# Optimization experiments

Hardware: AMD Instinct MI355X
Metric: run time of the kernel (lower is better)

The kernel has to match this reference:

```python
import jax, jax.numpy as jnp
import numpy as np

HEADS = 12
DIM_HEAD = 64
SCALE = DIM_HEAD ** -0.5


def setup_inputs() -> dict:
    key = jax.random.key(0)
    ks = jax.random.split(key, 5)
    b, n, dim = 16, 1024, 768
    inner = HEADS * DIM_HEAD  # 768
    x = jax.random.normal(ks[0], (b, n, dim), dtype=jnp.float32)
    w_qv = jax.random.normal(ks[1], (dim, 2 * inner), dtype=jnp.float32) * (dim ** -0.5)
    ext_k = jax.random.normal(ks[2], (1, HEADS, n, DIM_HEAD), dtype=jnp.float32)
    ext_bias = jax.random.normal(ks[3], (1, HEADS, n, n), dtype=jnp.float32)
    w_out = jax.random.normal(ks[4], (inner, dim), dtype=jnp.float32) * (inner ** -0.5)
    b_out = jnp.zeros((dim,), dtype=jnp.float32)
    return {"x": x, "w_qv": w_qv, "ext_k": ext_k, "ext_bias": ext_bias,
            "w_out": w_out, "b_out": b_out}


def reference(x, w_qv, ext_k, ext_bias, w_out, b_out):
    b, n, _ = x.shape
    qv = x @ w_qv                                   # [b, n, 2*inner]
    q, v = jnp.split(qv, 2, axis=-1)
    # b n (h d) -> b h n d
    q = q.reshape(b, n, HEADS, DIM_HEAD).transpose(0, 2, 1, 3)
    v = v.reshape(b, n, HEADS, DIM_HEAD).transpose(0, 2, 1, 3)
    # dots = (q @ ext_k^T + ext_bias) * scale       # [b, h, n, n]
    dots = (jnp.einsum('bhnd,ohmd->bhnm', q, ext_k) + ext_bias) * SCALE
    attn = jax.nn.softmax(dots, axis=-1)
    out = jnp.einsum('bhnm,bhmd->bhnd', attn, v)    # [b, h, n, d]
    out = out.transpose(0, 2, 1, 3).reshape(b, n, HEADS * DIM_HEAD)
    return out @ w_out + b_out
```

## Files before the change

kernel.cpp:

```cpp
#include <hip/hip_runtime.h>
#include <hip/hip_bf16.h>
#include <stdint.h>

typedef __bf16 bf16;
typedef short  s16x8 __attribute__((ext_vector_type(8)));
typedef float  f32x4 __attribute__((ext_vector_type(4)));

#define NHEADS  12
#define QKSCALE 0.125f

__device__ __forceinline__ void gload_lds16(const void* g, void* l) {
  __builtin_amdgcn_global_load_lds(
      (__attribute__((address_space(1))) void*)(g),
      (__attribute__((address_space(3))) void*)(l), 16, 0, 0);
}

__device__ __forceinline__ short bf16bits(float f) {
  union { bf16 h; short s; } u;
  u.h = (bf16)f;
  return u.s;
}
__device__ __forceinline__ float bfu2f(unsigned short u) {
  union { unsigned int i; float f; } c;
  c.i = ((unsigned int)u) << 16;
  return c.f;
}

__global__ __launch_bounds__(256) void cast4_kernel(const float* __restrict__ in,
                                                    bf16* __restrict__ out,
                                                    int n4, float scale) {
  int i = blockIdx.x * 256 + threadIdx.x;
  if (i >= n4) return;
  float4 v = ((const float4*)in)[i];
  union { bf16 h[4]; uint64_t u; } o;
  o.h[0] = (bf16)(v.x * scale);
  o.h[1] = (bf16)(v.y * scale);
  o.h[2] = (bf16)(v.z * scale);
  o.h[3] = (bf16)(v.w * scale);
  ((uint64_t*)out)[i] = o.u;
}

__global__ __launch_bounds__(256) void castT_tiled(const float* __restrict__ in,
                                                   bf16* __restrict__ out,
                                                   int R, int C) {
  __shared__ float tile[32][33];
  const int nbx = C >> 5;
  const int bx = blockIdx.x % nbx, by = blockIdx.x / nbx;
  const int tx = threadIdx.x & 31, ty = threadIdx.x >> 5;
  const int r0 = by << 5, c0 = bx << 5;
#pragma unroll
  for (int i = 0; i < 4; ++i)
    tile[ty + i * 8][tx] = in[(size_t)(r0 + ty + i * 8) * C + c0 + tx];
  __syncthreads();
#pragma unroll
  for (int i = 0; i < 4; ++i)
    out[(size_t)(c0 + ty + i * 8) * R + r0 + tx] = (bf16)tile[tx][ty + i * 8];
}

template <int EPI>
__global__ __launch_bounds__(256) void gemm128(const bf16* __restrict__ A,
                                               const bf16* __restrict__ BT,
                                               int M, int N, int K,
                                               bf16* __restrict__ outQ,
                                               bf16* __restrict__ outVT,
                                               float* __restrict__ outC,
                                               const float* __restrict__ bias) {
  __shared__ char sA[2][8192];
  __shared__ char sB[2][8192];
  const int cpx = gridDim.x >> 3;
  const int orig = blockIdx.x;
  const int blk = (orig & 7) * cpx + (orig >> 3);
  const int nb = N >> 7;
  const int bx = blk % nb, by = blk / nb;
  const int brow = by << 7, bcol = bx << 7;
  const int t = threadIdx.x;
  const int w = t >> 6, l = t & 63;
  const int wr = w >> 1, wc = w & 1;
  const int lr = l & 15, lg = l >> 4;

  const f32x4 fz = {0.f, 0.f, 0.f, 0.f};
  f32x4 acc[4][4];
#pragma unroll
  for (int m = 0; m < 4; ++m)
#pragma unroll
    for (int n = 0; n < 4; ++n) acc[m][n] = fz;

#define G_STAGE(kt_, buf_)                                                     \
  {                                                                            \
    _Pragma("unroll") for (int i = 0; i < 2; ++i) {                            \
      int chunk = ((i * 4 + w) << 6) + l;                                      \
      int rrow = chunk >> 2, rc = chunk & 3;                                   \
      gload_lds16(A + (size_t)(brow + rrow) * K + ((kt_) << 5) + (rc << 3),    \
                  sA[buf_] + ((i * 4 + w) << 10));                             \
      gload_lds16(BT + (size_t)(bcol + rrow) * K + ((kt_) << 5) + (rc << 3),   \
                  sB[buf_] + ((i * 4 + w) << 10));                             \
    }                                                                          \
  }

  const int nk = K >> 5;
  G_STAGE(0, 0);
  __syncthreads();
  for (int kt = 0; kt < nk; ++kt) {
    const int cur = kt & 1, nxt = cur ^ 1;
    if (kt + 1 < nk) G_STAGE(kt + 1, nxt);
    s16x8 af[4], bfr[4];
#pragma unroll
    for (int m = 0; m < 4; ++m)
      af[m] = *(const s16x8*)(sA[cur] + ((wr << 6) + (m << 4) + lr) * 64 + (lg << 4));
#pragma unroll
    for (int n = 0; n < 4; ++n)
      bfr[n] = *(const s16x8*)(sB[cur] + ((wc << 6) + (n << 4) + lr) * 64 + (lg << 4));
    __builtin_amdgcn_s_setprio(1);
#pragma unroll
    for (int m = 0; m < 4; ++m)
#pragma unroll
      for (int n = 0; n < 4; ++n)
        acc[m][n] = __builtin_amdgcn_mfma_f32_16x16x32_bf16(af[m], bfr[n], acc[m][n], 0, 0, 0);
    __builtin_amdgcn_s_setprio(0);
    __syncthreads();
  }
#undef G_STAGE

  if (EPI == 0) {
#pragma unroll
    for (int n = 0; n < 4; ++n) {
      int gcol = bcol + (wc << 6) + (n << 4) + lr;
      if (gcol < 768) {
        int h = gcol >> 6, d = gcol & 63;
#pragma unroll
        for (int m = 0; m < 4; ++m) {
          int growb = brow + (wr << 6) + (m << 4) + (lg << 2);
#pragma unroll
          for (int r = 0; r < 4; ++r) {
            int grow = growb + r;
            int b = grow >> 10, nr = grow & 1023;
            outQ[(((size_t)(b * NHEADS + h) << 10) + nr) * 64 + d] =
                (bf16)(acc[m][n][r] * QKSCALE);
          }
        }
      } else {
        int c2 = gcol - 768;
        int h = c2 >> 6, d = c2 & 63;
#pragma unroll
        for (int m = 0; m < 4; ++m) {
          int growb = brow + (wr << 6) + (m << 4) + (lg << 2);
          int b = growb >> 10, nr0 = growb & 1023;
          ushort4 pk;
          pk.x = (unsigned short)bf16bits(acc[m][n][0]);
          pk.y = (unsigned short)bf16bits(acc[m][n][1]);
          pk.z = (unsigned short)bf16bits(acc[m][n][2]);
          pk.w = (unsigned short)bf16bits(acc[m][n][3]);
          *(ushort4*)(outVT + ((((size_t)(b * NHEADS + h) << 6) + d) << 10) + nr0) = pk;
        }
      }
    }
  } else {
#pragma unroll
    for (int n = 0; n < 4; ++n) {
      int gcol = bcol + (wc << 6) + (n << 4) + lr;
      float bv = bias[gcol];
#pragma unroll
      for (int m = 0; m < 4; ++m) {
        int growb = brow + (wr << 6) + (m << 4) + (lg << 2);
#pragma unroll
        for (int r = 0; r < 4; ++r)
          outC[(size_t)(growb + r) * N + gcol] = acc[m][n][r] + bv;
      }
    }
  }
}

__global__ __launch_bounds__(256) void attn_kernel(const bf16* __restrict__ Q,
                                                   const bf16* __restrict__ VT,
                                                   const bf16* __restrict__ Kx,
                                                   const bf16* __restrict__ Bias,
                                                   bf16* __restrict__ O) {
  __shared__ char sK[2][8192];
  __shared__ char sVT[2][8192];
  __shared__ char sP[4][4096];

  const int cpx = gridDim.x >> 3;
  const int orig = blockIdx.x;
  const int blk = (orig & 7) * cpx + (orig >> 3);

  const int b  = blk & 15;
  const int qb = (blk >> 4) & 7;
  const int h  = blk >> 7;
  const int bh = b * NHEADS + h;
  const int t = threadIdx.x, w = t >> 6, l = t & 63;
  const int lr = l & 15, lg = l >> 4;
  const int q0 = (qb << 7) + (w << 5);
  const size_t qvbase = (size_t)bh << 10;

  s16x8 qf[2][2];
#pragma unroll
  for (int qg = 0; qg < 2; ++qg)
#pragma unroll
    for (int kf = 0; kf < 2; ++kf)
      qf[qg][kf] = *(const s16x8*)(Q + ((qvbase + q0 + (qg << 4) + lr) << 6) +
                                   (kf << 5) + (lg << 3));

  const f32x4 fz = {0.f, 0.f, 0.f, 0.f};
  f32x4 acc_o[2][4];
#pragma unroll
  for (int qg = 0; qg < 2; ++qg)
#pragma unroll
    for (int of = 0; of < 4; ++of) acc_o[qg][of] = fz;
  float lsum[2] = {0.f, 0.f};

  const bf16* Kh = Kx + ((size_t)h << 16);
  const bf16* Brow0 = Bias + ((size_t)((h << 10) + q0 + lr)) * 1024;
  const bf16* Brow1 = Brow0 + (16 << 10);
  const bf16* Vth = VT + (qvbase << 6);

#define STAGE_K(kt_, buf_)                                                  \
  {                                                                         \
    _Pragma("unroll") for (int i = 0; i < 2; ++i) {                         \
      int rowloc = ((i * 4 + w) << 3) + (l >> 3);                           \
      int chunk = (l & 7) ^ (rowloc & 7);                                   \
      gload_lds16(Kh + ((((kt_) << 6) + rowloc) << 6) + (chunk << 3),       \
                  sK[buf_] + ((i * 4 + w) << 10));                          \
    }                                                                       \
  }
#define STAGE_VT(kt_, buf_)                                                 \
  {                                                                         \
    _Pragma("unroll") for (int i = 0; i < 2; ++i) {                         \
      int rowloc = ((i * 4 + w) << 3) + (l >> 3);          \
      int chunk = (l & 7) ^ (rowloc & 7);                                   \
      gload_lds16(Vth + ((size_t)rowloc << 10) + ((kt_) << 6) + (chunk << 3), \
                  sVT[buf_] + ((i * 4 + w) << 10));                         \
    }                                                                       \
  }

  STAGE_K(0, 0);
  STAGE_VT(0, 0);
  ushort4 bu[2][4];
#pragma unroll
  for (int cf = 0; cf < 4; ++cf) {
    bu[0][cf] = *(const ushort4*)(Brow0 + (cf << 4) + (lg << 2));
    bu[1][cf] = *(const ushort4*)(Brow1 + (cf << 4) + (lg << 2));
  }
  __syncthreads();

  for (int kt = 0; kt < 16; ++kt) {
    const int cur = kt & 1, nxt = cur ^ 1;
    if (kt < 15) {
      STAGE_K(kt + 1, nxt);
      STAGE_VT(kt + 1, nxt);
    }

    f32x4 s[2][4];
#pragma unroll
    for (int qg = 0; qg < 2; ++qg)
#pragma unroll
      for (int cf = 0; cf < 4; ++cf) {
        s[qg][cf][0] = bfu2f(bu[qg][cf].x);
        s[qg][cf][1] = bfu2f(bu[qg][cf].y);
        s[qg][cf][2] = bfu2f(bu[qg][cf].z);
        s[qg][cf][3] = bfu2f(bu[qg][cf].w);
      }
    __builtin_amdgcn_s_setprio(1);
#pragma unroll
    for (int cf = 0; cf < 4; ++cf) {
      int kvloc = (cf << 4) + lr;
#pragma unroll
      for (int kf = 0; kf < 2; ++kf) {
        int chunk = ((kf << 2) + lg) ^ (kvloc & 7);
        s16x8 kb8 = *(const s16x8*)(sK[cur] + (kvloc << 7) + (chunk << 4));
        s[0][cf] = __builtin_amdgcn_mfma_f32_16x16x32_bf16(kb8, qf[0][kf], s[0][cf], 0, 0, 0);
        s[1][cf] = __builtin_amdgcn_mfma_f32_16x16x32_bf16(kb8, qf[1][kf], s[1][cf], 0, 0, 0);
      }
    }
    __builtin_amdgcn_s_setprio(0);

#pragma unroll
    for (int qg = 0; qg < 2; ++qg) {
      float psum = 0.f;
#pragma unroll
      for (int cf = 0; cf < 4; ++cf)
#pragma unroll
        for (int r = 0; r < 4; ++r) {
          float p = __expf(s[qg][cf][r]);
          s[qg][cf][r] = p;
          psum += p;
        }
      lsum[qg] += psum;
    }

#pragma unroll
    for (int qg = 0; qg < 2; ++qg)
#pragma unroll
      for (int cf = 0; cf < 4; ++cf) {
        ushort4 pk;
        pk.x = (unsigned short)bf16bits(s[qg][cf][0]);
        pk.y = (unsigned short)bf16bits(s[qg][cf][1]);
        pk.z = (unsigned short)bf16bits(s[qg][cf][2]);
        pk.w = (unsigned short)bf16bits(s[qg][cf][3]);
        int kvbyte = (cf << 5) + (lg << 3);
        int off = (qg << 11) + (lr << 7) +
                  ((((kvbyte >> 4) ^ (lr & 7)) << 4) | (kvbyte & 15));
        *(ushort4*)(sP[w] + off) = pk;
      }
    s16x8 pa[2][2];
#pragma unroll
    for (int qg = 0; qg < 2; ++qg)
#pragma unroll
      for (int kf2 = 0; kf2 < 2; ++kf2) {
        int chunk = ((kf2 << 2) + lg) ^ (lr & 7);
        pa[qg][kf2] = *(const s16x8*)(sP[w] + (qg << 11) + (lr << 7) + (chunk << 4));
      }

    if (kt < 15) {
#pragma unroll
      for (int cf = 0; cf < 4; ++cf) {
        bu[0][cf] = *(const ushort4*)(Brow0 + ((kt + 1) << 6) + (cf << 4) + (lg << 2));
        bu[1][cf] = *(const ushort4*)(Brow1 + ((kt + 1) << 6) + (cf << 4) + (lg << 2));
      }
    }

    __builtin_amdgcn_s_setprio(1);
#pragma unroll
    for (int of = 0; of < 4; ++of) {
      int d = (of << 4) + lr;
#pragma unroll
      for (int kf2 = 0; kf2 < 2; ++kf2) {
        int chunk = ((kf2 << 2) + lg) ^ (d & 7);
        s16x8 vbf = *(const s16x8*)(sVT[cur] + (d << 7) + (chunk << 4));
        acc_o[0][of] = __builtin_amdgcn_mfma_f32_16x16x32_bf16(pa[0][kf2], vbf, acc_o[0][of], 0, 0, 0);
        acc_o[1][of] = __builtin_amdgcn_mfma_f32_16x16x32_bf16(pa[1][kf2], vbf, acc_o[1][of], 0, 0, 0);
      }
    }
    __builtin_amdgcn_s_setprio(0);

    __syncthreads();
  }

  const int bb = b;
#pragma unroll
  for (int qg = 0; qg < 2; ++qg) {
    float ls = lsum[qg];
    ls += __shfl_xor(ls, 16);
    ls += __shfl_xor(ls, 32);
    float inv[4];
#pragma unroll
    for (int r = 0; r < 4; ++r)
      inv[r] = 1.0f / __shfl(ls, (lg << 4) + (lg << 2) + r);
#pragma unroll
    for (int of = 0; of < 4; ++of)
#pragma unroll
      for (int r = 0; r < 4; ++r) {
        int qrow = q0 + (qg << 4) + (lg << 2) + r;
        size_t off = ((size_t)((bb << 10) + qrow)) * 768 + (h << 6) + (of << 4) + lr;
        O[off] = (bf16)(acc_o[qg][of][r] * inv[r]);
      }
  }
#undef STAGE_K
#undef STAGE_VT
}

extern "C" void kernel_launch(void* const* d_in, const int* in_sizes, int n_in,
                              void* d_out, int out_size, void* d_ws, size_t ws_size,
                              hipStream_t stream) {
  const float* x        = (const float*)d_in[0];
  const float* w_qv     = (const float*)d_in[1];
  const float* ext_k    = (const float*)d_in[2];
  const float* ext_bias = (const float*)d_in[3];
  const float* w_out    = (const float*)d_in[4];
  const float* b_out    = (const float*)d_in[5];
  float* out = (float*)d_out;

  char* ws = (char*)d_ws;
  bf16* xb    = (bf16*)(ws);
  bf16* wqvT  = (bf16*)(ws + 25165824);
  bf16* kb    = (bf16*)(ws + 27525120);
  bf16* wobT  = (bf16*)(ws + 29097984);
  bf16* biasb = (bf16*)(ws + 30277632);
  bf16* qws   = (bf16*)(ws + 55443456);
  bf16* vtws  = (bf16*)(ws + 80609280);
  bf16* attout = xb;

  cast4_kernel<<<12288, 256, 0, stream>>>(x, xb, 3145728, 1.0f);
  cast4_kernel<<<12288, 256, 0, stream>>>(ext_bias, biasb, 3145728, QKSCALE);
  cast4_kernel<<<768, 256, 0, stream>>>(ext_k, kb, 196608, 1.0f);
  castT_tiled<<<1152, 256, 0, stream>>>(w_qv, wqvT, 768, 1536);
  castT_tiled<<<576, 256, 0, stream>>>(w_out, wobT, 768, 768);

  gemm128<0><<<1536, 256, 0, stream>>>(xb, wqvT, 16384, 1536, 768, qws, vtws, nullptr, nullptr);
  attn_kernel<<<1536, 256, 0, stream>>>(qws, vtws, kb, biasb, attout);
  gemm128<1><<<768, 256, 0, stream>>>(attout, wobT, 16384, 768, 768, nullptr, nullptr, out, b_out);
}
```

Measured before the change: 381.7 us.

## Merge cast kernels into one launch and enlarge GEMM tile to 256x128

```diff
diff --git a/kernel.cpp b/kernel.cpp
--- a/kernel.cpp
+++ b/kernel.cpp
@@ -26,73 +26,95 @@
   return c.f;
 }
 
-__global__ __launch_bounds__(256) void cast4_kernel(const float* __restrict__ in,
-                                                    bf16* __restrict__ out,
-                                                    int n4, float scale) {
-  int i = blockIdx.x * 256 + threadIdx.x;
-  if (i >= n4) return;
-  float4 v = ((const float4*)in)[i];
-  union { bf16 h[4]; uint64_t u; } o;
-  o.h[0] = (bf16)(v.x * scale);
-  o.h[1] = (bf16)(v.y * scale);
-  o.h[2] = (bf16)(v.z * scale);
-  o.h[3] = (bf16)(v.w * scale);
-  ((uint64_t*)out)[i] = o.u;
-}
-
-__global__ __launch_bounds__(256) void castT_tiled(const float* __restrict__ in,
-                                                   bf16* __restrict__ out,
-                                                   int R, int C) {
+__global__ __launch_bounds__(256) void prep_kernel(const float* __restrict__ x,
+                                                   const float* __restrict__ bias,
+                                                   const float* __restrict__ k,
+                                                   const float* __restrict__ wqv,
+                                                   const float* __restrict__ wout,
+                                                   bf16* __restrict__ xb,
+                                                   bf16* __restrict__ biasb,
+                                                   bf16* __restrict__ kb,
+                                                   bf16* __restrict__ wqvT,
+                                                   bf16* __restrict__ woutT) {
   __shared__ float tile[32][33];
-  const int nbx = C >> 5;
-  const int bx = blockIdx.x % nbx, by = blockIdx.x / nbx;
-  const int tx = threadIdx.x & 31, ty = threadIdx.x >> 5;
-  const int r0 = by << 5, c0 = bx << 5;
-#pragma unroll
-  for (int i = 0; i < 4; ++i)
-    tile[ty + i * 8][tx] = in[(size_t)(r0 + ty + i * 8) * C + c0 + tx];
-  __syncthreads();
-#pragma unroll
-  for (int i = 0; i < 4; ++i)
-    out[(size_t)(c0 + ty + i * 8) * R + r0 + tx] = (bf16)tile[tx][ty + i * 8];
+  const int blk = blockIdx.x;
+  if (blk < 25344) {
+    const float* in;
+    bf16* out;
+    int i;
+    float scale = 1.0f;
+    if (blk < 12288) {
+      in = x; out = xb; i = blk * 256 + threadIdx.x;
+    } else if (blk < 24576) {
+      in = bias; out = biasb; i = (blk - 12288) * 256 + threadIdx.x; scale = QKSCALE;
+    } else {
+      in = k; out = kb; i = (blk - 24576) * 256 + threadIdx.x;
+    }
+    float4 v = ((const float4*)in)[i];
+    union { bf16 h[4]; uint64_t u; } o;
+    o.h[0] = (bf16)(v.x * scale);
+    o.h[1] = (bf16)(v.y * scale);
+    o.h[2] = (bf16)(v.z * scale);
+    o.h[3] = (bf16)(v.w * scale);
+    ((uint64_t*)out)[i] = o.u;
+  } else {
+    const float* in;
+    bf16* out;
+    int rel, R, C;
+    if (blk < 26496) { in = wqv; out = wqvT; rel = blk - 25344; R = 768; C = 1536; }
+    else             { in = wout; out = woutT; rel = blk - 26496; R = 768; C = 768; }
+    const int nbx = C >> 5;
+    const int bx = rel % nbx, by = rel / nbx;
+    const int tx = threadIdx.x & 31, ty = threadIdx.x >> 5;
+    const int r0 = by << 5, c0 = bx << 5;
+#pragma unroll
+    for (int i = 0; i < 4; ++i)
+      tile[ty + i * 8][tx] = in[(size_t)(r0 + ty + i * 8) * C + c0 + tx];
+    __syncthreads();
+#pragma unroll
+    for (int i = 0; i < 4; ++i)
+      out[(size_t)(c0 + ty + i * 8) * R + r0 + tx] = (bf16)tile[tx][ty + i * 8];
+  }
 }
 
 template <int EPI>
-__global__ __launch_bounds__(256) void gemm128(const bf16* __restrict__ A,
-                                               const bf16* __restrict__ BT,
-                                               int M, int N, int K,
-                                               bf16* __restrict__ outQ,
-                                               bf16* __restrict__ outVT,
-                                               float* __restrict__ outC,
-                                               const float* __restrict__ bias) {
-  __shared__ char sA[2][8192];
+__global__ __launch_bounds__(256, 2) void gemm256(const bf16* __restrict__ A,
+                                                  const bf16* __restrict__ BT,
+                                                  int M, int N, int K,
+                                                  bf16* __restrict__ outQ,
+                                                  bf16* __restrict__ outVT,
+                                                  float* __restrict__ outC,
+                                                  const float* __restrict__ bias) {
+  __shared__ char sA[2][16384];
   __shared__ char sB[2][8192];
   const int cpx = gridDim.x >> 3;
   const int orig = blockIdx.x;
   const int blk = (orig & 7) * cpx + (orig >> 3);
   const int nb = N >> 7;
   const int bx = blk % nb, by = blk / nb;
-  const int brow = by << 7, bcol = bx << 7;
+  const int brow = by << 8, bcol = bx << 7;
   const int t = threadIdx.x;
   const int w = t >> 6, l = t & 63;
   const int wr = w >> 1, wc = w & 1;
   const int lr = l & 15, lg = l >> 4;
 
   const f32x4 fz = {0.f, 0.f, 0.f, 0.f};
-  f32x4 acc[4][4];
-#pragma unroll
-  for (int m = 0; m < 4; ++m)
+  f32x4 acc[8][4];
+#pragma unroll
+  for (int m = 0; m < 8; ++m)
 #pragma unroll
     for (int n = 0; n < 4; ++n) acc[m][n] = fz;
 
 #define G_STAGE(kt_, buf_)                                                     \
   {                                                                            \
+    _Pragma("unroll") for (int i = 0; i < 4; ++i) {                            \
+      int c = ((i * 4 + w) << 6) + l;                                          \
+      gload_lds16(A + (size_t)(brow + (c >> 2)) * K + ((kt_) << 5) + ((c & 3) << 3), \
+                  sA[buf_] + ((i * 4 + w) << 10));                             \
+    }                                                                          \
     _Pragma("unroll") for (int i = 0; i < 2; ++i) {                            \
-      int chunk = ((i * 4 + w) << 6) + l;                                      \
-      int rrow = chunk >> 2, rc = chunk & 3;                                   \
-      gload_lds16(A + (size_t)(brow + rrow) * K + ((kt_) << 5) + (rc << 3),    \
-                  sA[buf_] + ((i * 4 + w) << 10));                             \
-      gload_lds16(BT + (size_t)(bcol + rrow) * K + ((kt_) << 5) + (rc << 3),   \
+      int c = ((i * 4 + w) << 6) + l;                                          \
+      gload_lds16(BT + (size_t)(bcol + (c >> 2)) * K + ((kt_) << 5) + ((c & 3) << 3), \
                   sB[buf_] + ((i * 4 + w) << 10));                             \
     }                                                                          \
   }
@@ -103,33 +125,32 @@
   for (int kt = 0; kt < nk; ++kt) {
     const int cur = kt & 1, nxt = cur ^ 1;
     if (kt + 1 < nk) G_STAGE(kt + 1, nxt);
-    s16x8 af[4], bfr[4];
-#pragma unroll
-    for (int m = 0; m < 4; ++m)
-      af[m] = *(const s16x8*)(sA[cur] + ((wr << 6) + (m << 4) + lr) * 64 + (lg << 4));
+    s16x8 bfr[4];
 #pragma unroll
     for (int n = 0; n < 4; ++n)
       bfr[n] = *(const s16x8*)(sB[cur] + ((wc << 6) + (n << 4) + lr) * 64 + (lg << 4));
     __builtin_amdgcn_s_setprio(1);
 #pragma unroll
-    for (int m = 0; m < 4; ++m)
+    for (int m = 0; m < 8; ++m) {
+      s16x8 af = *(const s16x8*)(sA[cur] + ((wr << 7) + (m << 4) + lr) * 64 + (lg << 4));
 #pragma unroll
       for (int n = 0; n < 4; ++n)
-        acc[m][n] = __builtin_amdgcn_mfma_f32_16x16x32_bf16(af[m], bfr[n], acc[m][n], 0, 0, 0);
+        acc[m][n] = __builtin_amdgcn_mfma_f32_16x16x32_bf16(af, bfr[n], acc[m][n], 0, 0, 0);
+    }
     __builtin_amdgcn_s_setprio(0);
     __syncthreads();
   }
 #undef G_STAGE
 
   if (EPI == 0) {
-#pragma unroll
-    for (int n = 0; n < 4; ++n) {
-      int gcol = bcol + (wc << 6) + (n << 4) + lr;
-      if (gcol < 768) {
+    if (bcol < 768) {
+#pragma unroll
+      for (int n = 0; n < 4; ++n) {
+        int gcol = bcol + (wc << 6) + (n << 4) + lr;
         int h = gcol >> 6, d = gcol & 63;
 #pragma unroll
-        for (int m = 0; m < 4; ++m) {
-          int growb = brow + (wr << 6) + (m << 4) + (lg << 2);
+        for (int m = 0; m < 8; ++m) {
+          int growb = brow + (wr << 7) + (m << 4) + (lg << 2);
 #pragma unroll
           for (int r = 0; r < 4; ++r) {
             int grow = growb + r;
@@ -138,12 +159,15 @@
                 (bf16)(acc[m][n][r] * QKSCALE);
           }
         }
-      } else {
-        int c2 = gcol - 768;
+      }
+    } else {
+#pragma unroll
+      for (int n = 0; n < 4; ++n) {
+        int c2 = bcol - 768 + (wc << 6) + (n << 4) + lr;
         int h = c2 >> 6, d = c2 & 63;
 #pragma unroll
-        for (int m = 0; m < 4; ++m) {
-          int growb = brow + (wr << 6) + (m << 4) + (lg << 2);
+        for (int m = 0; m < 8; ++m) {
+          int growb = brow + (wr << 7) + (m << 4) + (lg << 2);
           int b = growb >> 10, nr0 = growb & 1023;
           ushort4 pk;
           pk.x = (unsigned short)bf16bits(acc[m][n][0]);
@@ -160,8 +184,8 @@
       int gcol = bcol + (wc << 6) + (n << 4) + lr;
       float bv = bias[gcol];
 #pragma unroll
-      for (int m = 0; m < 4; ++m) {
-        int growb = brow + (wr << 6) + (m << 4) + (lg << 2);
+      for (int m = 0; m < 8; ++m) {
+        int growb = brow + (wr << 7) + (m << 4) + (lg << 2);
 #pragma unroll
         for (int r = 0; r < 4; ++r)
           outC[(size_t)(growb + r) * N + gcol] = acc[m][n][r] + bv;
@@ -335,7 +359,6 @@
     __syncthreads();
   }
 
-  const int bb = b;
 #pragma unroll
   for (int qg = 0; qg < 2; ++qg) {
     float ls = lsum[qg];
@@ -350,7 +373,7 @@
 #pragma unroll
       for (int r = 0; r < 4; ++r) {
         int qrow = q0 + (qg << 4) + (lg << 2) + r;
-        size_t off = ((size_t)((bb << 10) + qrow)) * 768 + (h << 6) + (of << 4) + lr;
+        size_t off = ((size_t)((b << 10) + qrow)) * 768 + (h << 6) + (of << 4) + lr;
         O[off] = (bf16)(acc_o[qg][of][r] * inv[r]);
       }
   }
@@ -379,13 +402,10 @@
   bf16* vtws  = (bf16*)(ws + 80609280);
   bf16* attout = xb;
 
-  cast4_kernel<<<12288, 256, 0, stream>>>(x, xb, 3145728, 1.0f);
-  cast4_kernel<<<12288, 256, 0, stream>>>(ext_bias, biasb, 3145728, QKSCALE);
-  cast4_kernel<<<768, 256, 0, stream>>>(ext_k, kb, 196608, 1.0f);
-  castT_tiled<<<1152, 256, 0, stream>>>(w_qv, wqvT, 768, 1536);
-  castT_tiled<<<576, 256, 0, stream>>>(w_out, wobT, 768, 768);
-
-  gemm128<0><<<1536, 256, 0, stream>>>(xb, wqvT, 16384, 1536, 768, qws, vtws, nullptr, nullptr);
+  prep_kernel<<<27072, 256, 0, stream>>>(x, ext_bias, ext_k, w_qv, w_out,
+                                         xb, biasb, kb, wqvT, wobT);
+
+  gemm256<0><<<768, 256, 0, stream>>>(xb, wqvT, 16384, 1536, 768, qws, vtws, nullptr, nullptr);
   attn_kernel<<<1536, 256, 0, stream>>>(qws, vtws, kb, biasb, attout);
-  gemm128<1><<<768, 256, 0, stream>>>(attout, wobT, 16384, 768, 768, nullptr, nullptr, out, b_out);
-}
+  gemm256<1><<<384, 256, 0, stream>>>(attout, wobT, 16384, 768, 768, nullptr, nullptr, out, b_out);
+}
```

After: 378.6 us. About the same (-0.8%).
